# Kernel tuning notes

Hardware: AMD Instinct MI355X
Metric: run time of the kernel (lower is better)

## Reference

```python
import jax, jax.numpy as jnp
import numpy as np

D = 256   # model dim
M = 64    # num mechanisms
B = 4
S = 8192


def setup_inputs() -> dict:
    key = jax.random.key(0)
    ks = jax.random.split(key, 16)
    n = jax.random.normal
    inp = {
        "x": n(ks[0], (B, S, D), jnp.float32),
        "context": n(ks[1], (B, S, D), jnp.float32),
        # stacked per-mechanism params (m, out, in) etc.
        "Wm": n(ks[2], (M, D, D), jnp.float32) * (1.0 / np.sqrt(D)),
        "bm": n(ks[3], (M, D), jnp.float32) * 0.02,
        "cm": n(ks[4], (M, D), jnp.float32),           # characteristics (1,1,dim) per node
        "um": n(ks[5], (M, D), jnp.float32) * (1.0 / np.sqrt(D)),  # timing_gate weight
        "vm": n(ks[6], (M,), jnp.float32) * 0.02,       # timing_gate bias
        # selector: Linear(d, 2d) -> GELU -> Linear(2d, m)
        "W1": n(ks[7], (2 * D, D), jnp.float32) * (1.0 / np.sqrt(D)),
        "b1": n(ks[8], (2 * D,), jnp.float32) * 0.02,
        "W2": n(ks[9], (M, 2 * D), jnp.float32) * (1.0 / np.sqrt(2 * D)),
        "b2": n(ks[10], (M,), jnp.float32) * 0.02,
        # integrate: Linear(2d, d)
        "Wi": n(ks[11], (D, 2 * D), jnp.float32) * (1.0 / np.sqrt(2 * D)),
        "bi": n(ks[12], (D,), jnp.float32) * 0.02,
    }
    return inp


def reference(x, context, Wm, bm, cm, um, vm, W1, b1, W2, b2, Wi, bi):
    # selector: softmax over mechanisms (b, s, m)
    h = jax.nn.gelu(jnp.einsum('bsd,ed->bse', context, W1) + b1, approximate=False)
    scores = jax.nn.softmax(jnp.einsum('bse,me->bsm', h, W2) + b2, axis=-1)

    # per-mechanism sigmoid timing gate (b, s, m)
    gate = jax.nn.sigmoid(jnp.einsum('bsd,md->bsm', x, um) + vm)

    # combined weight a[b,s,m] = softmax_score * gate; then
    # selected = sum_m a * (x @ Wm.T + bm + cm)  -- contracted without
    # materializing the (b, s, m, d) stack the torch loop builds.
    a = scores * gate                               # (b, s, m)
    selected = jnp.einsum('bsm,bse,mde->bsd', a, x, Wm) \
             + jnp.einsum('bsm,md->bsd', a, bm + cm)

    # integrate(concat([x, selected]))
    cat = jnp.concatenate([x, selected], axis=-1)   # (b, s, 2d)
    integrated = jnp.einsum('bse,de->bsd', cat, Wi) + bi
    return integrated
```

## Files before the change

kernel.cpp:

```cpp
#include <hip/hip_runtime.h>
#include <cstdint>
#include <cstddef>


typedef _Float16 f16;
typedef f16 f16x8 __attribute__((ext_vector_type(8)));
typedef float f32x4 __attribute__((ext_vector_type(4)));
typedef float f32x16 __attribute__((ext_vector_type(16)));

#define DEV __device__ __forceinline__

DEV uint32_t swz128(uint32_t b) { return b ^ (((b >> 7) & 7u) << 4); }

DEV void gload_lds16(const void* g, void* l) {
  __builtin_amdgcn_global_load_lds(
      (const __attribute__((address_space(1))) unsigned int*)g,
      (__attribute__((address_space(3))) unsigned int*)l, 16, 0, 0);
}

DEV f16x8 cvt8(float4 u0, float4 u1) {
  f16x8 v = {(f16)u0.x, (f16)u0.y, (f16)u0.z, (f16)u0.w,
             (f16)u1.x, (f16)u1.y, (f16)u1.z, (f16)u1.w};
  return v;
}

__global__ void prep_b_kernel(const float* __restrict__ S, f16* __restrict__ dst,
                              int K, int BN, int total) {
  int t = blockIdx.x * 256 + threadIdx.x;
  if (t >= total) return;
  int gpc = BN * 8;
  int g = t % gpc;
  int c = (t / gpc) % (K / 64);
  int cb = t / (gpc * (K / 64));
  int ks = g / (BN * 4);
  int rem = g % (BN * 4);
  int col = rem >> 2;
  int kg = rem & 3;
  int J = cb * BN + col;
  int k = c * 64 + ks * 32 + kg * 8;
  const float* s = S + (size_t)J * K + k;
  float4 u0 = *(const float4*)s;
  float4 u1 = *(const float4*)(s + 4);
  f16* chunk = dst + (size_t)(cb * (K / 64) + c) * (BN * 64);
  *(f16x8*)((char*)chunk + swz128((uint32_t)g * 16)) = cvt8(u0, u1);
}

__global__ void prep_wcat_kernel(const float* __restrict__ Wm,
                                 const float* __restrict__ bm,
                                 const float* __restrict__ cm,
                                 f16* __restrict__ dst) {
  int t = blockIdx.x * 256 + threadIdx.x;
  if (t >= 257 * 2048) return;
  int g = t & 2047;
  int c = t >> 11;
  int kstep = g >> 9;
  int khalf = (g >> 8) & 1;
  int col = g & 255;
  int k0 = kstep * 16 + khalf * 8;
  f16x8 v;
  if (c < 256) {
    int m = c & 63;
    int e0 = (c >> 6) * 64 + k0;
    const float* s = Wm + ((size_t)m * 256 + col) * 256 + e0;
    float4 u0 = *(const float4*)s;
    float4 u1 = *(const float4*)(s + 4);
    v = cvt8(u0, u1);
  } else {
#pragma unroll
    for (int j = 0; j < 8; ++j) {
      int k = k0 + j;
      v[j] = (f16)(bm[k * 256 + col] + cm[k * 256 + col]);
    }
  }
  *(f16x8*)(dst + (size_t)c * 16384 + (size_t)g * 8) = v;
}

template <int BN, int NCHUNK, int A0C, int EPI>
__global__ __launch_bounds__(BN == 256 ? 512 : 256, 2)
void gemm_tpl(const float* __restrict__ A0, int lda0,
              const f16* __restrict__ A1, int lda1,
              const f16* __restrict__ Bt,
              const float* __restrict__ bias,
              float* __restrict__ outF, f16* __restrict__ outH, int ldo) {
  constexpr int WAVES = (BN == 256) ? 8 : 4;
  constexpr int THREADS = WAVES * 64;
  constexpr int WC = (BN == 256) ? 4 : 1;
  constexpr int WR = WAVES / WC;
  constexpr int RT = 128 / (WR * 16);
  constexpr int CT = (BN / WC) / 16;

  __shared__ alignas(16) f16 sA[2][128 * 64];
  __shared__ alignas(16) f16 sB[2][BN * 64];

  const int tid = threadIdx.x;
  const int lane = tid & 63;
  const int wid = tid >> 6;
  const int wr = wid / WC, wc = wid % WC;
  const int rb = blockIdx.x, cb = blockIdx.y;

  auto stageB = [&](int c, int buf) {
    const char* src = (const char*)(Bt + (size_t)(cb * NCHUNK + c) * (BN * 64));
#pragma unroll
    for (int it = 0; it < (BN * 64 * 2) / (THREADS * 16); ++it) {
      int off = (it * THREADS + tid) * 16;
      gload_lds16(src + off, (char*)&sB[buf][0] + off);
    }
  };
  auto stageA = [&](int c, int buf) {
#pragma unroll
    for (int it = 0; it < 1024 / THREADS; ++it) {
      int gg = it * THREADS + tid;
      int row = gg >> 3, eg = gg & 7;
      size_t rowG = (size_t)rb * 128 + row;
      f16x8 v;
      if (A0C > 0 && c < A0C) {
        const float* s = A0 + rowG * lda0 + c * 64 + eg * 8;
        float4 u0 = *(const float4*)s;
        float4 u1 = *(const float4*)(s + 4);
        v = cvt8(u0, u1);
      } else {
        v = *(const f16x8*)(A1 + rowG * lda1 + (c - A0C) * 64 + eg * 8);
      }
      *(f16x8*)((char*)&sA[buf][0] + swz128((uint32_t)(row * 128 + eg * 16))) = v;
    }
  };

  f32x4 acc[RT][CT];
#pragma unroll
  for (int i = 0; i < RT; ++i)
#pragma unroll
    for (int j = 0; j < CT; ++j) acc[i][j] = (f32x4){0.f, 0.f, 0.f, 0.f};

  stageB(0, 0);
  stageA(0, 0);
  __syncthreads();

  for (int c = 0; c < NCHUNK; ++c) {
    int cur = c & 1;
    if (c + 1 < NCHUNK) {
      stageB(c + 1, cur ^ 1);
      stageA(c + 1, cur ^ 1);
    }
#pragma unroll
    for (int ks = 0; ks < 2; ++ks) {
      f16x8 af[RT], bf[CT];
#pragma unroll
      for (int rt = 0; rt < RT; ++rt) {
        int row = wr * (RT * 16) + rt * 16 + (lane & 15);
        af[rt] = *(const f16x8*)((const char*)&sA[cur][0] +
                                 swz128((uint32_t)(row * 128 + ks * 64 + (lane >> 4) * 16)));
      }
#pragma unroll
      for (int ct = 0; ct < CT; ++ct) {
        int col = wc * (CT * 16) + ct * 16 + (lane & 15);
        bf[ct] = *(const f16x8*)((const char*)&sB[cur][0] +
                                 swz128((uint32_t)(((ks * BN + col) * 4 + (lane >> 4)) * 16)));
      }
#pragma unroll
      for (int rt = 0; rt < RT; ++rt)
#pragma unroll
        for (int ct = 0; ct < CT; ++ct)
          acc[rt][ct] = __builtin_amdgcn_mfma_f32_16x16x32_f16(af[rt], bf[ct], acc[rt][ct], 0, 0, 0);
    }
    __syncthreads();
  }

#pragma unroll
  for (int rt = 0; rt < RT; ++rt)
#pragma unroll
    for (int ct = 0; ct < CT; ++ct)
#pragma unroll
      for (int i = 0; i < 4; ++i) {
        size_t row = (size_t)rb * 128 + wr * (RT * 16) + rt * 16 + (lane >> 4) * 4 + i;
        int colG = cb * BN + wc * (CT * 16) + ct * 16 + (lane & 15);
        float v = acc[rt][ct][i];
        if constexpr (EPI == 0) {
          if (bias) v += bias[colG];
          outF[row * ldo + colG] = v;
        } else {
          v += bias[colG];
          float ge = 0.5f * v * (1.0f + erff(v * 0.70710678118f));
          outH[row * ldo + colG] = (f16)ge;
        }
      }
}

__global__ void selector_finish(const float* __restrict__ logits,
                                const float* __restrict__ glog,
                                const float* __restrict__ b2,
                                const float* __restrict__ vm,
                                f16* __restrict__ a16) {
  int n = blockIdx.x * 4 + (threadIdx.x >> 6);
  int m = threadIdx.x & 63;
  float l = logits[(size_t)n * 64 + m] + b2[m];
  float mx = l;
#pragma unroll
  for (int o = 32; o; o >>= 1) mx = fmaxf(mx, __shfl_xor(mx, o));
  float p = expf(l - mx);
  float s = p;
#pragma unroll
  for (int o = 32; o; o >>= 1) s += __shfl_xor(s, o);
  float g = glog[(size_t)n * 64 + m] + vm[m];
  float gate = 1.0f / (1.0f + expf(-g));
  a16[(size_t)n * 64 + m] = (f16)(p / s * gate);
}

__global__ __launch_bounds__(512, 2)
void big_gemm(const float* __restrict__ x, const f16* __restrict__ a16,
              const f16* __restrict__ Wcat, f16* __restrict__ sel) {
  __shared__ alignas(16) f16 sB[4][256 * 64];
  __shared__ alignas(16) f16 sAa[128 * 72];

  const int tid = threadIdx.x;
  const int lane = tid & 63;
  const int wid = tid >> 6;
  const int l31 = lane & 31;
  const int khalf = lane >> 5;
  const int rb = blockIdx.x;

  auto stageB = [&](int c, int buf) {
    const char* src = (const char*)(Wcat + (size_t)c * 16384);
#pragma unroll
    for (int it = 0; it < 4; ++it) {
      int off = (it * 512 + tid) * 16;
      gload_lds16(src + off, (char*)&sB[buf][0] + off);
    }
  };

#pragma unroll
  for (int it = 0; it < 2; ++it) {
    int gg = it * 512 + tid;
    int row = gg >> 3, mg = gg & 7;
    f16x8 v = *(const f16x8*)(a16 + ((size_t)rb * 128 + row) * 64 + mg * 8);
    *(f16x8*)((char*)sAa + row * 144 + mg * 16) = v;
  }
  stageB(0, 0);
  stageB(1, 1);
  stageB(2, 2);
  asm volatile("s_waitcnt vmcnt(8) lgkmcnt(0)" ::: "memory");
  __builtin_amdgcn_s_barrier();
  __builtin_amdgcn_sched_barrier(0);

  f32x16 acc[4];
#pragma unroll
  for (int rt = 0; rt < 4; ++rt)
#pragma unroll
    for (int r = 0; r < 16; ++r) acc[rt][r] = 0.f;

  f16x8 xv[4][4];
  auto loadXV = [&](int er) {
#pragma unroll
    for (int rt = 0; rt < 4; ++rt)
#pragma unroll
      for (int ks = 0; ks < 4; ++ks) {
        const float* s = x + ((size_t)rb * 128 + rt * 32 + l31) * 256
                           + er * 64 + ks * 16 + khalf * 8;
        float4 u0 = *(const float4*)s;
        float4 u1 = *(const float4*)(s + 4);
        xv[rt][ks] = cvt8(u0, u1);
      }
  };

  const int bOff = khalf * 4096 + wid * 512 + l31 * 16;

  f16x8 bf[2][4];
#pragma unroll
  for (int ks = 0; ks < 4; ++ks)
    bf[0][ks] = *(const f16x8*)((const char*)&sB[0][0] + bOff + ks * 8192);

  for (int q8 = 0; q8 < 256; q8 += 8) {
    if ((q8 & 63) == 0) loadXV(q8 >> 6);
    f16x8 as8[4];
#pragma unroll
    for (int rt = 0; rt < 4; ++rt)
      as8[rt] = *(const f16x8*)((const char*)sAa + (rt * 32 + l31) * 144 + (q8 & 63) * 2);
#pragma unroll
    for (int u = 0; u < 8; ++u) {
      const int q = q8 + u;
      asm volatile("s_waitcnt vmcnt(4)" ::: "memory");
      __builtin_amdgcn_s_barrier();
      __builtin_amdgcn_sched_barrier(0);
      stageB(q + 3, (u + 3) & 3);
      const char* nb = (const char*)&sB[(u + 1) & 3][0] + bOff;
#pragma unroll
      for (int ks = 0; ks < 4; ++ks)
        bf[(u + 1) & 1][ks] = *(const f16x8*)(nb + ks * 8192);
      __builtin_amdgcn_s_setprio(1);
#pragma unroll
      for (int ks = 0; ks < 4; ++ks) {
#pragma unroll
        for (int rt = 0; rt < 4; ++rt) {
          f16x8 af = xv[rt][ks] * as8[rt][u];
          acc[rt] = __builtin_amdgcn_mfma_f32_32x32x16_f16(af, bf[u & 1][ks], acc[rt], 0, 0, 0);
        }
      }
      __builtin_amdgcn_s_setprio(0);
    }
  }

#pragma unroll
  for (int ks = 0; ks < 4; ++ks) {
#pragma unroll
    for (int rt = 0; rt < 4; ++rt) {
      f16x8 af = *(const f16x8*)((const char*)sAa + (rt * 32 + l31) * 144
                                 + ks * 32 + khalf * 16);
      acc[rt] = __builtin_amdgcn_mfma_f32_32x32x16_f16(af, bf[0][ks], acc[rt], 0, 0, 0);
    }
  }

#pragma unroll
  for (int rt = 0; rt < 4; ++rt)
#pragma unroll
    for (int r = 0; r < 16; ++r) {
      int rowin = (r & 3) + 8 * (r >> 2) + 4 * khalf;
      size_t row = (size_t)rb * 128 + rt * 32 + rowin;
      sel[row * 256 + wid * 32 + l31] = (f16)acc[rt][r];
    }
}

extern "C" void kernel_launch(void* const* d_in, const int* in_sizes, int n_in,
                              void* d_out, int out_size, void* d_ws, size_t ws_size,
                              hipStream_t stream) {
  (void)in_sizes; (void)n_in; (void)out_size;
  const float* x   = (const float*)d_in[0];
  const float* ctx = (const float*)d_in[1];
  const float* Wm  = (const float*)d_in[2];
  const float* bm  = (const float*)d_in[3];
  const float* cm  = (const float*)d_in[4];
  const float* um  = (const float*)d_in[5];
  const float* vm  = (const float*)d_in[6];
  const float* W1  = (const float*)d_in[7];
  const float* b1  = (const float*)d_in[8];
  const float* W2  = (const float*)d_in[9];
  const float* b2  = (const float*)d_in[10];
  const float* Wi  = (const float*)d_in[11];
  const float* bi  = (const float*)d_in[12];
  float* out = (float*)d_out;

  char* ws = (char*)d_ws;
  size_t off = 0;
  f16* Wcat = (f16*)(ws + off); off += (size_t)260 * 16384 * 2;
  f16* W1t  = (f16*)(ws + off); off += (size_t)512 * 256 * 2;
  f16* W2t  = (f16*)(ws + off); off += (size_t)64 * 512 * 2;
  f16* umt  = (f16*)(ws + off); off += (size_t)64 * 256 * 2;
  f16* Wit  = (f16*)(ws + off); off += (size_t)256 * 512 * 2;
  f16* h16  = (f16*)(ws + off); off += (size_t)32768 * 512 * 2;
  float* logits = (float*)(ws + off); off += (size_t)32768 * 64 * 4;
  float* glog   = (float*)(ws + off); off += (size_t)32768 * 64 * 4;
  f16* a16   = (f16*)(ws + off); off += (size_t)32768 * 64 * 2;
  f16* sel16 = (f16*)(ws + off); off += (size_t)32768 * 256 * 2;
  if (ws_size < off) return;

  prep_wcat_kernel<<<dim3(257 * 2048 / 256), dim3(256), 0, stream>>>(Wm, bm, cm, Wcat);
  prep_b_kernel<<<dim3(16384 / 256), dim3(256), 0, stream>>>(W1, W1t, 256, 256, 16384);
  prep_b_kernel<<<dim3(4096 / 256),  dim3(256), 0, stream>>>(W2, W2t, 512, 64, 4096);
  prep_b_kernel<<<dim3(2048 / 256),  dim3(256), 0, stream>>>(um, umt, 256, 64, 2048);
  prep_b_kernel<<<dim3(16384 / 256), dim3(256), 0, stream>>>(Wi, Wit, 512, 256, 16384);

  gemm_tpl<256, 4, 4, 1><<<dim3(256, 2), dim3(512), 0, stream>>>(
      ctx, 256, nullptr, 0, W1t, b1, nullptr, h16, 512);
  gemm_tpl<64, 4, 4, 0><<<dim3(256, 1), dim3(256), 0, stream>>>(
      x, 256, nullptr, 0, umt, nullptr, glog, nullptr, 64);
  gemm_tpl<64, 8, 0, 0><<<dim3(256, 1), dim3(256), 0, stream>>>(
      nullptr, 0, h16, 512, W2t, nullptr, logits, nullptr, 64);
  selector_finish<<<dim3(32768 / 4), dim3(256), 0, stream>>>(logits, glog, b2, vm, a16);

  big_gemm<<<dim3(256), dim3(512), 0, stream>>>(x, a16, Wcat, sel16);

  gemm_tpl<256, 8, 4, 0><<<dim3(256, 1), dim3(512), 0, stream>>>(
      x, 256, sel16, 256, Wit, bi, out, nullptr, 256);
}
```

Measured before the change: 388.0 us.

## Split big_gemm output columns across two blocks with 2x2 wave tiling

The mechanism-contraction GEMM is split into two column halves, giving 512 blocks of 256 threads instead of 256 blocks of 512 threads. Each wave now computes a 64x64 tile (2x2 MFMA tiles) rather than 128x32. The Wcat prep layout is re-chunked per column half, and the LDS B buffering drops from four to three stages with rotating pointers. The aim is more blocks for better CU occupancy and less LDS per block, at the cost of each block re-reading x and re-applying the per-row scale for its half.

```diff
diff --git a/kernel.cpp b/kernel.cpp
--- a/kernel.cpp
+++ b/kernel.cpp
@@ -50,12 +50,13 @@
                                  const float* __restrict__ cm,
                                  f16* __restrict__ dst) {
   int t = blockIdx.x * 256 + threadIdx.x;
-  if (t >= 257 * 2048) return;
-  int g = t & 2047;
-  int c = t >> 11;
-  int kstep = g >> 9;
-  int khalf = (g >> 8) & 1;
-  int col = g & 255;
+  if (t >= 2 * 257 * 1024) return;
+  int g = t & 1023;
+  int c = (t >> 10) % 257;
+  int cb = t / (257 * 1024);
+  int kstep = g >> 8;
+  int khalf = (g >> 7) & 1;
+  int col = cb * 128 + (g & 127);
   int k0 = kstep * 16 + khalf * 8;
   f16x8 v;
   if (c < 256) {
@@ -72,7 +73,7 @@
       v[j] = (f16)(bm[k * 256 + col] + cm[k * 256 + col]);
     }
   }
-  *(f16x8*)(dst + (size_t)c * 16384 + (size_t)g * 8) = v;
+  *(f16x8*)(dst + ((size_t)(cb * 260 + c)) * 8192 + (size_t)g * 8) = v;
 }
 
 template <int BN, int NCHUNK, int A0C, int EPI>
@@ -205,55 +206,70 @@
   a16[(size_t)n * 64 + m] = (f16)(p / s * gate);
 }
 
-__global__ __launch_bounds__(512, 2)
+__global__ __launch_bounds__(256, 2)
 void big_gemm(const float* __restrict__ x, const f16* __restrict__ a16,
               const f16* __restrict__ Wcat, f16* __restrict__ sel) {
-  __shared__ alignas(16) f16 sB[4][256 * 64];
+  __shared__ alignas(16) f16 sB[3][128 * 64];
   __shared__ alignas(16) f16 sAa[128 * 72];
 
   const int tid = threadIdx.x;
   const int lane = tid & 63;
   const int wid = tid >> 6;
+  const int wr = wid >> 1, wc = wid & 1;
   const int l31 = lane & 31;
   const int khalf = lane >> 5;
-  const int rb = blockIdx.x;
-
-  auto stageB = [&](int c, int buf) {
-    const char* src = (const char*)(Wcat + (size_t)c * 16384);
+  const int rb = blockIdx.x, cb = blockIdx.y;
+  const f16* Wb = Wcat + (size_t)cb * 260 * 8192;
+
+  auto stageTo = [&](int c, char* dstLds) {
+    const char* src = (const char*)(Wb + (size_t)c * 8192);
 #pragma unroll
     for (int it = 0; it < 4; ++it) {
-      int off = (it * 512 + tid) * 16;
-      gload_lds16(src + off, (char*)&sB[buf][0] + off);
+      int off = (it * 256 + tid) * 16;
+      gload_lds16(src + off, dstLds + off);
     }
   };
 
 #pragma unroll
-  for (int it = 0; it < 2; ++it) {
-    int gg = it * 512 + tid;
+  for (int it = 0; it < 4; ++it) {
+    int gg = it * 256 + tid;
     int row = gg >> 3, mg = gg & 7;
     f16x8 v = *(const f16x8*)(a16 + ((size_t)rb * 128 + row) * 64 + mg * 8);
     *(f16x8*)((char*)sAa + row * 144 + mg * 16) = v;
   }
-  stageB(0, 0);
-  stageB(1, 1);
-  stageB(2, 2);
-  asm volatile("s_waitcnt vmcnt(8) lgkmcnt(0)" ::: "memory");
+  char* p0 = (char*)&sB[0][0];
+  char* p1 = (char*)&sB[1][0];
+  char* p2 = (char*)&sB[2][0];
+  stageTo(0, p0);
+  stageTo(1, p1);
+  asm volatile("s_waitcnt vmcnt(4) lgkmcnt(0)" ::: "memory");
   __builtin_amdgcn_s_barrier();
   __builtin_amdgcn_sched_barrier(0);
 
-  f32x16 acc[4];
-#pragma unroll
-  for (int rt = 0; rt < 4; ++rt)
-#pragma unroll
-    for (int r = 0; r < 16; ++r) acc[rt][r] = 0.f;
-
-  f16x8 xv[4][4];
+  const int bOff = khalf * 2048 + wc * 1024 + l31 * 16;
+
+  f32x16 acc[2][2];
+#pragma unroll
+  for (int i = 0; i < 2; ++i)
+#pragma unroll
+    for (int j = 0; j < 2; ++j)
+#pragma unroll
+      for (int r = 0; r < 16; ++r) acc[i][j][r] = 0.f;
+
+  f16x8 bf[2][8];
+#pragma unroll
+  for (int ks = 0; ks < 4; ++ks)
+#pragma unroll
+    for (int ct = 0; ct < 2; ++ct)
+      bf[0][ks * 2 + ct] = *(const f16x8*)(p0 + bOff + ks * 4096 + ct * 512);
+
+  f16x8 xv[2][4];
   auto loadXV = [&](int er) {
 #pragma unroll
-    for (int rt = 0; rt < 4; ++rt)
+    for (int rt = 0; rt < 2; ++rt)
 #pragma unroll
       for (int ks = 0; ks < 4; ++ks) {
-        const float* s = x + ((size_t)rb * 128 + rt * 32 + l31) * 256
+        const float* s = x + ((size_t)rb * 128 + wr * 64 + rt * 32 + l31) * 256
                            + er * 64 + ks * 16 + khalf * 8;
         float4 u0 = *(const float4*)s;
         float4 u1 = *(const float4*)(s + 4);
@@ -261,61 +277,62 @@
       }
   };
 
-  const int bOff = khalf * 4096 + wid * 512 + l31 * 16;
-
-  f16x8 bf[2][4];
-#pragma unroll
-  for (int ks = 0; ks < 4; ++ks)
-    bf[0][ks] = *(const f16x8*)((const char*)&sB[0][0] + bOff + ks * 8192);
-
   for (int q8 = 0; q8 < 256; q8 += 8) {
     if ((q8 & 63) == 0) loadXV(q8 >> 6);
-    f16x8 as8[4];
-#pragma unroll
-    for (int rt = 0; rt < 4; ++rt)
-      as8[rt] = *(const f16x8*)((const char*)sAa + (rt * 32 + l31) * 144 + (q8 & 63) * 2);
+    f16x8 as8[2];
+#pragma unroll
+    for (int rt = 0; rt < 2; ++rt)
+      as8[rt] = *(const f16x8*)((const char*)sAa + (wr * 64 + rt * 32 + l31) * 144 + (q8 & 63) * 2);
 #pragma unroll
     for (int u = 0; u < 8; ++u) {
       const int q = q8 + u;
+      stageTo(q + 2, p2);
       asm volatile("s_waitcnt vmcnt(4)" ::: "memory");
       __builtin_amdgcn_s_barrier();
       __builtin_amdgcn_sched_barrier(0);
-      stageB(q + 3, (u + 3) & 3);
-      const char* nb = (const char*)&sB[(u + 1) & 3][0] + bOff;
+      const char* nb = p1 + bOff;
 #pragma unroll
       for (int ks = 0; ks < 4; ++ks)
-        bf[(u + 1) & 1][ks] = *(const f16x8*)(nb + ks * 8192);
+#pragma unroll
+        for (int ct = 0; ct < 2; ++ct)
+          bf[(u + 1) & 1][ks * 2 + ct] = *(const f16x8*)(nb + ks * 4096 + ct * 512);
       __builtin_amdgcn_s_setprio(1);
 #pragma unroll
-      for (int ks = 0; ks < 4; ++ks) {
-#pragma unroll
-        for (int rt = 0; rt < 4; ++rt) {
+      for (int ks = 0; ks < 4; ++ks)
+#pragma unroll
+        for (int rt = 0; rt < 2; ++rt) {
           f16x8 af = xv[rt][ks] * as8[rt][u];
-          acc[rt] = __builtin_amdgcn_mfma_f32_32x32x16_f16(af, bf[u & 1][ks], acc[rt], 0, 0, 0);
+#pragma unroll
+          for (int ct = 0; ct < 2; ++ct)
+            acc[rt][ct] = __builtin_amdgcn_mfma_f32_32x32x16_f16(af, bf[u & 1][ks * 2 + ct], acc[rt][ct], 0, 0, 0);
         }
-      }
       __builtin_amdgcn_s_setprio(0);
+      char* t = p0; p0 = p1; p1 = p2; p2 = t;
     }
   }
 
 #pragma unroll
-  for (int ks = 0; ks < 4; ++ks) {
-#pragma unroll
-    for (int rt = 0; rt < 4; ++rt) {
-      f16x8 af = *(const f16x8*)((const char*)sAa + (rt * 32 + l31) * 144
+  for (int ks = 0; ks < 4; ++ks)
+#pragma unroll
+    for (int rt = 0; rt < 2; ++rt) {
+      f16x8 af = *(const f16x8*)((const char*)sAa + (wr * 64 + rt * 32 + l31) * 144
                                  + ks * 32 + khalf * 16);
-      acc[rt] = __builtin_amdgcn_mfma_f32_32x32x16_f16(af, bf[0][ks], acc[rt], 0, 0, 0);
-    }
-  }
-
-#pragma unroll
-  for (int rt = 0; rt < 4; ++rt)
-#pragma unroll
-    for (int r = 0; r < 16; ++r) {
-      int rowin = (r & 3) + 8 * (r >> 2) + 4 * khalf;
-      size_t row = (size_t)rb * 128 + rt * 32 + rowin;
-      sel[row * 256 + wid * 32 + l31] = (f16)acc[rt][r];
-    }
+#pragma unroll
+      for (int ct = 0; ct < 2; ++ct)
+        acc[rt][ct] = __builtin_amdgcn_mfma_f32_32x32x16_f16(af, bf[0][ks * 2 + ct], acc[rt][ct], 0, 0, 0);
+    }
+
+#pragma unroll
+  for (int rt = 0; rt < 2; ++rt)
+#pragma unroll
+    for (int ct = 0; ct < 2; ++ct)
+#pragma unroll
+      for (int r = 0; r < 16; ++r) {
+        int rowin = (r & 3) + 8 * (r >> 2) + 4 * khalf;
+        size_t row = (size_t)rb * 128 + wr * 64 + rt * 32 + rowin;
+        int col = cb * 128 + wc * 64 + ct * 32 + l31;
+        sel[row * 256 + col] = (f16)acc[rt][ct][r];
+      }
 }
 
 extern "C" void kernel_launch(void* const* d_in, const int* in_sizes, int n_in,
@@ -339,7 +356,7 @@
 
   char* ws = (char*)d_ws;
   size_t off = 0;
-  f16* Wcat = (f16*)(ws + off); off += (size_t)260 * 16384 * 2;
+  f16* Wcat = (f16*)(ws + off); off += (size_t)2 * 260 * 8192 * 2;
   f16* W1t  = (f16*)(ws + off); off += (size_t)512 * 256 * 2;
   f16* W2t  = (f16*)(ws + off); off += (size_t)64 * 512 * 2;
   f16* umt  = (f16*)(ws + off); off += (size_t)64 * 256 * 2;
@@ -351,7 +368,7 @@
   f16* sel16 = (f16*)(ws + off); off += (size_t)32768 * 256 * 2;
   if (ws_size < off) return;
 
-  prep_wcat_kernel<<<dim3(257 * 2048 / 256), dim3(256), 0, stream>>>(Wm, bm, cm, Wcat);
+  prep_wcat_kernel<<<dim3(2056), dim3(256), 0, stream>>>(Wm, bm, cm, Wcat);
   prep_b_kernel<<<dim3(16384 / 256), dim3(256), 0, stream>>>(W1, W1t, 256, 256, 16384);
   prep_b_kernel<<<dim3(4096 / 256),  dim3(256), 0, stream>>>(W2, W2t, 512, 64, 4096);
   prep_b_kernel<<<dim3(2048 / 256),  dim3(256), 0, stream>>>(um, umt, 256, 64, 2048);
@@ -365,7 +382,7 @@
       nullptr, 0, h16, 512, W2t, nullptr, logits, nullptr, 64);
   selector_finish<<<dim3(32768 / 4), dim3(256), 0, stream>>>(logits, glog, b2, vm, a16);
 
-  big_gemm<<<dim3(256), dim3(512), 0, stream>>>(x, a16, Wcat, sel16);
+  big_gemm<<<dim3(256, 2), dim3(256), 0, stream>>>(x, a16, Wcat, sel16);
 
   gemm_tpl<256, 8, 4, 0><<<dim3(256, 1), dim3(512), 0, stream>>>(
       x, 256, sel16, 256, Wit, bi, out, nullptr, 256);
```

Result: faster. 355.2 us (-8.4%).
